# Kernel tuning notes

Measured on AMD Instinct MI355X. Metric: run time of the kernel, lower is better.

## Reference

```python
import jax, jax.numpy as jnp
import numpy as np

NUM_Q = 8      # num_quantizers
D = 1024       # input feature dim
CDIM = 32      # factorized codebook dim
K = 1024       # codebook_size
B = 16
T = 4096
COMMIT = 0.25  # commitment loss weight


def setup_inputs() -> dict:
    key = jax.random.key(0)
    ks = jax.random.split(key, 4)
    x = jax.random.normal(ks[0], (B, D, T), jnp.float32)
    in_w = jax.random.normal(ks[1], (NUM_Q, CDIM, D), jnp.float32) / np.sqrt(D).astype(np.float32)
    in_b = jnp.zeros((NUM_Q, CDIM), jnp.float32)
    out_w = jax.random.normal(ks[2], (NUM_Q, D, CDIM), jnp.float32) / np.sqrt(CDIM).astype(np.float32)
    out_b = jnp.zeros((NUM_Q, D), jnp.float32)
    codebook = jax.random.normal(ks[3], (NUM_Q, K, CDIM), jnp.float32)
    return dict(x=x, in_w=in_w, in_b=in_b, out_w=out_w, out_b=out_b, codebook=codebook)


def _l2norm(v, axis):
    n = jnp.sqrt(jnp.sum(v * v, axis=axis, keepdims=True))
    return v / jnp.maximum(n, 1e-12)


def _fvq(residual, w_in, b_in, w_out, b_out, cb):
    # residual: [B, D, T] -> factorized latent [B, CDIM, T]
    z_e = jnp.einsum('cd,bdt->bct', w_in, residual) + b_in[None, :, None]
    enc = _l2norm(z_e, axis=1)          # normalize over channel dim
    cbn = _l2norm(cb, axis=-1)          # [K, CDIM]
    # with unit-norm vectors, argmin(L2 dist) == argmax(cosine sim)
    sim = jnp.einsum('bct,kc->btk', enc, cbn)   # [B, T, K]
    idx = jnp.argmax(sim, axis=-1)              # [B, T] int
    z_q = jnp.transpose(cb[idx], (0, 2, 1))     # gather -> [B, CDIM, T]
    commit = jnp.mean((z_e - jax.lax.stop_gradient(z_q)) ** 2, axis=(1, 2))  # [B]
    codeb = jnp.mean((z_q - jax.lax.stop_gradient(z_e)) ** 2, axis=(1, 2))   # [B]
    loss = COMMIT * commit + codeb
    z_q = z_e + jax.lax.stop_gradient(z_q - z_e)  # straight-through estimator
    out = jnp.einsum('dc,bct->bdt', w_out, z_q) + b_out[None, :, None]
    return out, idx, loss


def reference(x, in_w, in_b, out_w, out_b, codebook):
    quantized_out = jnp.zeros_like(x)
    residual = x
    all_idx, all_loss = [], []
    for q in range(NUM_Q):  # fixed small stage count, sequential by construction
        z_q, idx, loss = _fvq(residual, in_w[q], in_b[q], out_w[q], out_b[q], codebook[q])
        quantized_out = quantized_out + z_q
        residual = residual - z_q
        all_idx.append(idx)
        all_loss.append(jnp.mean(loss))
    return quantized_out, jnp.stack(all_idx), jnp.stack(all_loss)
```

## Files before the change

kernel.cpp:

```cpp
#include <hip/hip_runtime.h>

#define NUM_Q 8
#define D     1024
#define CDIM  32
#define K     1024
#define B     16
#define T     4096
#define QC    (NUM_Q*CDIM)
#define EPSM  5e-4f

__global__ void k_cbn(const float* __restrict__ cb, double* __restrict__ cbn,
                      float* __restrict__ cbn32) {
  int i = blockIdx.x*blockDim.x + threadIdx.x;
  if (i >= NUM_Q*K) return;
  const float* v = cb + (size_t)i*CDIM;
  double s = 0.0;
  for (int c = 0; c < CDIM; ++c) { double x = (double)v[c]; s += x*x; }
  double n = sqrt(s);
  n = fmax(n, 1e-12);
  double* o = cbn + (size_t)i*CDIM;
  float*  o32 = cbn32 + (size_t)i*CDIM;
  for (int c = 0; c < CDIM; ++c) {
    double r = (double)v[c] / n;
    o[c] = r;
    o32[c] = (float)r;
  }
}

__global__ void k_prep(const float* __restrict__ out_b, double* __restrict__ obsum,
                       double* __restrict__ lossAcc) {
  int i = blockIdx.x*blockDim.x + threadIdx.x;
  if (i < NUM_Q) lossAcc[i] = 0.0;
  if (i < D) {
    double s = 0.0;
    for (int q = 0; q < NUM_Q; ++q) s += (double)out_b[q*D + i];
    obsum[i] = s;
  }
}

__global__ void k_w64(const float* __restrict__ in_w, double* __restrict__ w64t) {
  int i = blockIdx.x*blockDim.x + threadIdx.x;
  if (i < QC*D) {
    int j = i >> 10; int d = i & (D-1);
    w64t[(size_t)d*QC + j] = (double)in_w[i];
  }
}

__global__ void k_M(const float* __restrict__ in_w, const float* __restrict__ out_w,
                    const float* __restrict__ out_b, double* __restrict__ M,
                    double* __restrict__ vb) {
  int i = blockIdx.x*blockDim.x + threadIdx.x;
  int e = i & 31; int c = (i >> 5) & 31; int p = (i >> 10) & 7; int q = i >> 13;
  if (q >= NUM_Q) return;
  const float* wi = in_w + ((size_t)q*CDIM + c)*D;
  const float* wo = out_w + (size_t)p*D*CDIM + e;
  double s = 0.0;
  for (int d = 0; d < D; ++d) s += (double)wi[d] * (double)wo[(size_t)d*CDIM];
  M[i] = s;
  if (e == 0) {
    const float* ob = out_b + (size_t)p*D;
    double sb = 0.0;
    for (int d = 0; d < D; ++d) sb += (double)wi[d] * (double)ob[d];
    vb[(q*8 + p)*CDIM + c] = sb;
  }
}

__global__ void k_Mcb(const double* __restrict__ M, const float* __restrict__ cb,
                      double* __restrict__ Mcb) {
  long i = blockIdx.x*(long)blockDim.x + threadIdx.x;
  if (i >= (long)NUM_Q*NUM_Q*K*CDIM) return;
  int c = (int)(i & 31); long r = i >> 5;
  int k = (int)(r & (K-1)); r >>= 10;
  int p = (int)(r & 7); int q = (int)(r >> 3);
  if (q == 0 || p >= q) return;
  const double* m = M + (((size_t)(q*8 + p)*CDIM + c)*CDIM);
  const float* v = cb + ((size_t)p*K + k)*CDIM;
  double s = 0.0;
  for (int e = 0; e < CDIM; ++e) s += m[e] * (double)v[e];
  Mcb[((size_t)(q*8 + p)*K + k)*CDIM + c] = s;
}

__global__ __launch_bounds__(256, 4) void k_P(const float* __restrict__ x,
                                              const double* __restrict__ w64t,
                                              double* __restrict__ P) {
  int j0 = blockIdx.x*32;
  int t  = blockIdx.y*256 + threadIdx.x;
  int b  = blockIdx.z;
  double acc[32];
  #pragma unroll
  for (int j = 0; j < 32; ++j) acc[j] = 0.0;
  const float* xp = x + (size_t)b*D*T + t;
  float xb[4];
  #pragma unroll
  for (int u = 0; u < 4; ++u) xb[u] = xp[(size_t)u*T];
  for (int d0 = 0; d0 < D; d0 += 4) {
    float xn[4];
    if (d0 + 4 < D) {
      #pragma unroll
      for (int u = 0; u < 4; ++u) xn[u] = xp[(size_t)(d0 + 4 + u)*T];
    }
    #pragma unroll
    for (int u = 0; u < 4; ++u) {
      double xv = (double)xb[u];
      const double* wr = w64t + (size_t)(d0 + u)*QC + j0;
      #pragma unroll
      for (int jj = 0; jj < 32; ++jj) acc[jj] += xv * wr[jj];
    }
    #pragma unroll
    for (int u = 0; u < 4; ++u) xb[u] = xn[u];
  }
  double* Pp = P + ((size_t)b*QC + j0)*T + t;
  #pragma unroll
  for (int jj = 0; jj < 32; ++jj) Pp[(size_t)jj*T] = acc[jj];
}

__global__ __launch_bounds__(512, 4) void k_stage(
    int q,
    const double* __restrict__ P, const double* __restrict__ Mcb,
    const double* __restrict__ vb, const float* __restrict__ in_b,
    const double* __restrict__ cbn, const float* __restrict__ cbn32,
    const float* __restrict__ cb,
    int* __restrict__ idx_ws, float* __restrict__ zq,
    double* __restrict__ lossAcc, float* __restrict__ out_idx) {
  __shared__ double bs[4][128];
  __shared__ int    bkk[4][128];
  const int tt = threadIdx.x & 127;
  const int sg = (int)(__builtin_amdgcn_readfirstlane(threadIdx.x) >> 7);
  const int i  = blockIdx.x*128 + tt;
  const int b  = i >> 12;
  const int t  = i & (T-1);

  double z[CDIM];
  {
    const double* Pp = P + ((size_t)b*QC + q*CDIM)*T + t;
    #pragma unroll
    for (int c = 0; c < CDIM; ++c) z[c] = Pp[(size_t)c*T] + (double)in_b[q*CDIM + c];
  }
  for (int p = 0; p < q; ++p) {
    int kp = idx_ws[(size_t)p*B*T + i];
    const double* mc  = Mcb + ((size_t)(q*8 + p)*K + kp)*CDIM;
    const double* vbp = vb + (q*8 + p)*CDIM;
    #pragma unroll
    for (int c = 0; c < CDIM; ++c) z[c] -= (mc[c] + vbp[c]);
  }
  float zf[CDIM];
  #pragma unroll
  for (int c = 0; c < CDIM; ++c) zf[c] = (float)z[c];

  const float* c32 = cbn32 + ((size_t)q*K + (size_t)sg*(K/4))*CDIM;
  float best = -1e30f, second = -1e30f; int bi = 0;
  #pragma unroll 2
  for (int k = 0; k < K/4; ++k) {
    const float* r = c32 + (size_t)k*CDIM;
    float s0 = 0.f, s1 = 0.f, s2 = 0.f, s3 = 0.f;
    #pragma unroll
    for (int c = 0; c < CDIM; c += 4) {
      s0 += zf[c]*r[c]; s1 += zf[c+1]*r[c+1];
      s2 += zf[c+2]*r[c+2]; s3 += zf[c+3]*r[c+3];
    }
    float sim = (s0 + s1) + (s2 + s3);
    if (sim > best) { second = best; best = sim; bi = k; }
    else if (sim > second) { second = sim; }
  }

  const double* cbq = cbn + ((size_t)q*K + (size_t)sg*(K/4))*CDIM;
  double s64; int kwin = bi;
  if (best - second < EPSM) {
    double b64 = -1e300; int b64i = 0;
    for (int k = 0; k < K/4; ++k) {
      const double* r = cbq + (size_t)k*CDIM;
      double u0 = 0.0, u1 = 0.0, u2 = 0.0, u3 = 0.0;
      #pragma unroll
      for (int c = 0; c < CDIM; c += 4) {
        u0 += z[c]*r[c]; u1 += z[c+1]*r[c+1];
        u2 += z[c+2]*r[c+2]; u3 += z[c+3]*r[c+3];
      }
      double sd = (u0 + u1) + (u2 + u3);
      if (sd > b64) { b64 = sd; b64i = k; }
    }
    s64 = b64; kwin = b64i;
  } else {
    const double* r = cbq + (size_t)kwin*CDIM;
    double u0 = 0.0, u1 = 0.0, u2 = 0.0, u3 = 0.0;
    #pragma unroll
    for (int c = 0; c < CDIM; c += 4) {
      u0 += z[c]*r[c]; u1 += z[c+1]*r[c+1];
      u2 += z[c+2]*r[c+2]; u3 += z[c+3]*r[c+3];
    }
    s64 = (u0 + u1) + (u2 + u3);
  }
  bs[sg][tt]  = s64;
  bkk[sg][tt] = sg*(K/4) + kwin;
  __syncthreads();

  if (sg == 0) {
    double bb = bs[0][tt]; int kbest = bkk[0][tt];
    #pragma unroll
    for (int g = 1; g < 4; ++g) {
      if (bs[g][tt] > bb) { bb = bs[g][tt]; kbest = bkk[g][tt]; }
    }
    idx_ws[(size_t)q*B*T + i] = kbest;
    out_idx[(size_t)q*B*T + i] = (float)kbest;

    const float* cv = cb + ((size_t)q*K + kbest)*CDIM;
    float* zp = zq + ((size_t)b*QC + q*CDIM)*T + t;
    double l = 0.0;
    #pragma unroll
    for (int c = 0; c < CDIM; ++c) {
      float f = cv[c];
      zp[(size_t)c*T] = f;
      double d2 = z[c] - (double)f;
      l += d2*d2;
    }
    for (int off = 32; off > 0; off >>= 1) l += __shfl_down(l, off, 64);
    if ((threadIdx.x & 63) == 0) atomicAdd(&lossAcc[q], l);
  }
}

#define TT 4
__global__ __launch_bounds__(256) void k_out(const float* __restrict__ zq,
                                             const float* __restrict__ out_w,
                                             const double* __restrict__ obsum,
                                             float* __restrict__ out) {
  __shared__ float lw[QC][16];
  int d0 = blockIdx.x*16;
  int t0 = blockIdx.y*(256*TT);
  int b  = blockIdx.z;
  for (int u = threadIdx.x; u < 16*QC; u += 256) {
    int j = u >> 4; int a = u & 15;
    lw[j][a] = out_w[(size_t)(j >> 5)*D*CDIM + (size_t)(d0 + a)*CDIM + (j & 31)];
  }
  __syncthreads();
  float acc[16][TT];
  #pragma unroll
  for (int a = 0; a < 16; ++a)
    #pragma unroll
    for (int u = 0; u < TT; ++u) acc[a][u] = 0.f;
  const float* zp = zq + (size_t)b*QC*T + t0 + threadIdx.x;
  for (int j = 0; j < QC; ++j) {
    float zv[TT];
    #pragma unroll
    for (int u = 0; u < TT; ++u) zv[u] = zp[(size_t)j*T + u*256];
    #pragma unroll
    for (int a4 = 0; a4 < 4; ++a4) {
      float4 w = *(const float4*)&lw[j][a4*4];
      #pragma unroll
      for (int u = 0; u < TT; ++u) {
        acc[a4*4+0][u] += w.x*zv[u];
        acc[a4*4+1][u] += w.y*zv[u];
        acc[a4*4+2][u] += w.z*zv[u];
        acc[a4*4+3][u] += w.w*zv[u];
      }
    }
  }
  for (int a = 0; a < 16; ++a) {
    float bb = (float)obsum[d0 + a];
    float* op = out + ((size_t)b*D + d0 + a)*T + t0 + threadIdx.x;
    #pragma unroll
    for (int u = 0; u < TT; ++u) op[(size_t)u*256] = acc[a][u] + bb;
  }
}

__global__ void k_loss(const double* __restrict__ lossAcc, float* __restrict__ out_l) {
  int i = threadIdx.x;
  if (i < NUM_Q)
    out_l[i] = (float)(1.25 * lossAcc[i] / ((double)B * CDIM * T));
}

extern "C" void kernel_launch(void* const* d_in, const int* in_sizes, int n_in,
                              void* d_out, int out_size, void* d_ws, size_t ws_size,
                              hipStream_t stream) {
  const float* x     = (const float*)d_in[0];
  const float* in_w  = (const float*)d_in[1];
  const float* in_b  = (const float*)d_in[2];
  const float* out_w = (const float*)d_in[3];
  const float* out_b = (const float*)d_in[4];
  const float* cb    = (const float*)d_in[5];
  float* out = (float*)d_out;

  char* ws = (char*)d_ws;
  double* P    = (double*)(ws + 0);
  float*  zq   = (float*)(ws + 134217728);
  double* Mcb  = (double*)(ws + 201326592);
  double* cbn  = (double*)(ws + 218103808);
  double* M    = (double*)(ws + 220200960);
  int*    idxw = (int*)   (ws + 220725248);
  double* vb   = (double*)(ws + 222822400);
  double* obs  = (double*)(ws + 222838784);
  double* lac  = (double*)(ws + 222846976);
  double* w64t = Mcb;
  float*  cb32 = (float*)(ws + 203685888);

  float* out_q = out;
  float* out_i = out + 67108864;
  float* out_l = out + 67633152;

  k_cbn <<<dim3(32),  dim3(256), 0, stream>>>(cb, cbn, cb32);
  k_prep<<<dim3(4),   dim3(256), 0, stream>>>(out_b, obs, lac);
  k_w64 <<<dim3(1024),dim3(256), 0, stream>>>(in_w, w64t);
  k_M   <<<dim3(256), dim3(256), 0, stream>>>(in_w, out_w, out_b, M, vb);
  k_Mcb <<<dim3(8192),dim3(256), 0, stream>>>(M, cb, Mcb);
  k_P   <<<dim3(QC/32, T/256, B), dim3(256), 0, stream>>>(x, w64t, P);
  for (int q = 0; q < NUM_Q; ++q)
    k_stage<<<dim3(B*T/128), dim3(512), 0, stream>>>(q, P, Mcb, vb, in_b, cbn, cb32, cb,
                                                     idxw, zq, lac, out_i);
  k_out <<<dim3(D/16, T/(256*TT), B), dim3(256), 0, stream>>>(zq, out_w, obs, out_q);
  k_loss<<<dim3(1), dim3(64), 0, stream>>>(lac, out_l);
}
```

Before: 4.470 ms.

## Cut k_stage register pressure, fold vb into Mcb, and relayout k_P weights

In k_stage the double-precision latent is now built only briefly to produce the float copy, then rebuilt after the fp32 codebook scan, so 32 doubles no longer stay live through the hot loop. The cost is reloading P and the earlier-stage Mcb rows. The vb bias is pre-added into Mcb so the stage kernel skips those adds. k_P now reads in_w in its original row-major double layout with double2 loads over pairs of d, instead of a transposed layout. The near-tie threshold that triggers the fp64 re-scan is also widened, so the fallback runs more often.

```diff
diff --git a/kernel.cpp b/kernel.cpp
--- a/kernel.cpp
+++ b/kernel.cpp
@@ -7,7 +7,7 @@
 #define B     16
 #define T     4096
 #define QC    (NUM_Q*CDIM)
-#define EPSM  5e-4f
+#define EPSM  1e-3f
 
 __global__ void k_cbn(const float* __restrict__ cb, double* __restrict__ cbn,
                       float* __restrict__ cbn32) {
@@ -38,12 +38,9 @@
   }
 }
 
-__global__ void k_w64(const float* __restrict__ in_w, double* __restrict__ w64t) {
+__global__ void k_w64(const float* __restrict__ in_w, double* __restrict__ w64) {
   int i = blockIdx.x*blockDim.x + threadIdx.x;
-  if (i < QC*D) {
-    int j = i >> 10; int d = i & (D-1);
-    w64t[(size_t)d*QC + j] = (double)in_w[i];
-  }
+  if (i < QC*D) w64[i] = (double)in_w[i];
 }
 
 __global__ void k_M(const float* __restrict__ in_w, const float* __restrict__ out_w,
@@ -66,7 +63,7 @@
 }
 
 __global__ void k_Mcb(const double* __restrict__ M, const float* __restrict__ cb,
-                      double* __restrict__ Mcb) {
+                      const double* __restrict__ vb, double* __restrict__ Mcb) {
   long i = blockIdx.x*(long)blockDim.x + threadIdx.x;
   if (i >= (long)NUM_Q*NUM_Q*K*CDIM) return;
   int c = (int)(i & 31); long r = i >> 5;
@@ -75,13 +72,13 @@
   if (q == 0 || p >= q) return;
   const double* m = M + (((size_t)(q*8 + p)*CDIM + c)*CDIM);
   const float* v = cb + ((size_t)p*K + k)*CDIM;
-  double s = 0.0;
+  double s = vb[(q*8 + p)*CDIM + c];
   for (int e = 0; e < CDIM; ++e) s += m[e] * (double)v[e];
   Mcb[((size_t)(q*8 + p)*K + k)*CDIM + c] = s;
 }
 
 __global__ __launch_bounds__(256, 4) void k_P(const float* __restrict__ x,
-                                              const double* __restrict__ w64t,
+                                              const double* __restrict__ w64,
                                               double* __restrict__ P) {
   int j0 = blockIdx.x*32;
   int t  = blockIdx.y*256 + threadIdx.x;
@@ -90,24 +87,16 @@
   #pragma unroll
   for (int j = 0; j < 32; ++j) acc[j] = 0.0;
   const float* xp = x + (size_t)b*D*T + t;
-  float xb[4];
-  #pragma unroll
-  for (int u = 0; u < 4; ++u) xb[u] = xp[(size_t)u*T];
-  for (int d0 = 0; d0 < D; d0 += 4) {
-    float xn[4];
-    if (d0 + 4 < D) {
-      #pragma unroll
-      for (int u = 0; u < 4; ++u) xn[u] = xp[(size_t)(d0 + 4 + u)*T];
-    }
-    #pragma unroll
-    for (int u = 0; u < 4; ++u) {
-      double xv = (double)xb[u];
-      const double* wr = w64t + (size_t)(d0 + u)*QC + j0;
-      #pragma unroll
-      for (int jj = 0; jj < 32; ++jj) acc[jj] += xv * wr[jj];
-    }
-    #pragma unroll
-    for (int u = 0; u < 4; ++u) xb[u] = xn[u];
+  #pragma unroll 2
+  for (int d = 0; d < D; d += 2) {
+    double xv0 = (double)xp[(size_t)d*T];
+    double xv1 = (double)xp[(size_t)(d+1)*T];
+    #pragma unroll
+    for (int jj = 0; jj < 32; ++jj) {
+      double2 w = *(const double2*)(w64 + (size_t)(j0 + jj)*D + d);
+      acc[jj] += xv0 * w.x;
+      acc[jj] += xv1 * w.y;
+    }
   }
   double* Pp = P + ((size_t)b*QC + j0)*T + t;
   #pragma unroll
@@ -117,7 +106,7 @@
 __global__ __launch_bounds__(512, 4) void k_stage(
     int q,
     const double* __restrict__ P, const double* __restrict__ Mcb,
-    const double* __restrict__ vb, const float* __restrict__ in_b,
+    const float* __restrict__ in_b,
     const double* __restrict__ cbn, const float* __restrict__ cbn32,
     const float* __restrict__ cb,
     int* __restrict__ idx_ws, float* __restrict__ zq,
@@ -125,27 +114,27 @@
   __shared__ double bs[4][128];
   __shared__ int    bkk[4][128];
   const int tt = threadIdx.x & 127;
-  const int sg = (int)(__builtin_amdgcn_readfirstlane(threadIdx.x) >> 7);
+  const int sg = threadIdx.x >> 7;
   const int i  = blockIdx.x*128 + tt;
   const int b  = i >> 12;
   const int t  = i & (T-1);
 
-  double z[CDIM];
+  float zf[CDIM];
   {
+    double z[CDIM];
     const double* Pp = P + ((size_t)b*QC + q*CDIM)*T + t;
     #pragma unroll
     for (int c = 0; c < CDIM; ++c) z[c] = Pp[(size_t)c*T] + (double)in_b[q*CDIM + c];
-  }
-  for (int p = 0; p < q; ++p) {
-    int kp = idx_ws[(size_t)p*B*T + i];
-    const double* mc  = Mcb + ((size_t)(q*8 + p)*K + kp)*CDIM;
-    const double* vbp = vb + (q*8 + p)*CDIM;
-    #pragma unroll
-    for (int c = 0; c < CDIM; ++c) z[c] -= (mc[c] + vbp[c]);
-  }
-  float zf[CDIM];
-  #pragma unroll
-  for (int c = 0; c < CDIM; ++c) zf[c] = (float)z[c];
+    for (int p = 0; p < q; ++p) {
+      int kp = idx_ws[(size_t)p*B*T + i];
+      const double* mc = Mcb + ((size_t)(q*8 + p)*K + kp)*CDIM;
+      #pragma unroll
+      for (int c = 0; c < CDIM; ++c) z[c] -= mc[c];
+    }
+    #pragma unroll
+    for (int c = 0; c < CDIM; ++c) zf[c] = (float)z[c];
+  }
+  asm volatile("" ::: "memory");
 
   const float* c32 = cbn32 + ((size_t)q*K + (size_t)sg*(K/4))*CDIM;
   float best = -1e30f, second = -1e30f; int bi = 0;
@@ -161,6 +150,19 @@
     float sim = (s0 + s1) + (s2 + s3);
     if (sim > best) { second = best; best = sim; bi = k; }
     else if (sim > second) { second = sim; }
+  }
+
+  double z[CDIM];
+  {
+    const double* Pp = P + ((size_t)b*QC + q*CDIM)*T + t;
+    #pragma unroll
+    for (int c = 0; c < CDIM; ++c) z[c] = Pp[(size_t)c*T] + (double)in_b[q*CDIM + c];
+    for (int p = 0; p < q; ++p) {
+      int kp = idx_ws[(size_t)p*B*T + i];
+      const double* mc = Mcb + ((size_t)(q*8 + p)*K + kp)*CDIM;
+      #pragma unroll
+      for (int c = 0; c < CDIM; ++c) z[c] -= mc[c];
+    }
   }
 
   const double* cbq = cbn + ((size_t)q*K + (size_t)sg*(K/4))*CDIM;
@@ -288,7 +290,7 @@
   double* vb   = (double*)(ws + 222822400);
   double* obs  = (double*)(ws + 222838784);
   double* lac  = (double*)(ws + 222846976);
-  double* w64t = Mcb;
+  double* w64  = Mcb;
   float*  cb32 = (float*)(ws + 203685888);
 
   float* out_q = out;
@@ -297,12 +299,12 @@
 
   k_cbn <<<dim3(32),  dim3(256), 0, stream>>>(cb, cbn, cb32);
   k_prep<<<dim3(4),   dim3(256), 0, stream>>>(out_b, obs, lac);
-  k_w64 <<<dim3(1024),dim3(256), 0, stream>>>(in_w, w64t);
+  k_w64 <<<dim3(1024),dim3(256), 0, stream>>>(in_w, w64);
   k_M   <<<dim3(256), dim3(256), 0, stream>>>(in_w, out_w, out_b, M, vb);
-  k_Mcb <<<dim3(8192),dim3(256), 0, stream>>>(M, cb, Mcb);
-  k_P   <<<dim3(QC/32, T/256, B), dim3(256), 0, stream>>>(x, w64t, P);
+  k_Mcb <<<dim3(8192),dim3(256), 0, stream>>>(M, cb, vb, Mcb);
+  k_P   <<<dim3(QC/32, T/256, B), dim3(256), 0, stream>>>(x, w64, P);
   for (int q = 0; q < NUM_Q; ++q)
-    k_stage<<<dim3(B*T/128), dim3(512), 0, stream>>>(q, P, Mcb, vb, in_b, cbn, cb32, cb,
+    k_stage<<<dim3(B*T/128), dim3(512), 0, stream>>>(q, P, Mcb, in_b, cbn, cb32, cb,
                                                      idxw, zq, lac, out_i);
   k_out <<<dim3(D/16, T/(256*TT), B), dim3(256), 0, stream>>>(zq, out_w, obs, out_q);
   k_loss<<<dim3(1), dim3(64), 0, stream>>>(lac, out_l);
```

Result: slower. 5.699 ms (+27.5%).
